# Kernel tuning notes

Measured on AMD Instinct MI355X. Metric: run time of the kernel, lower is better.

## Reference

```python
import jax, jax.numpy as jnp
import numpy as np

N = 50000
E = 500000
IN_DIM = 384
HID = 64
HEADS = 4
OUT_DIM = 128
EPS_SM = 1e-16
EPS_LN = 1e-5
NEG_SLOPE = 0.2


def gat_conv(x, row, col, ew, W, a_src, a_dst, b, heads, out_ch, concat):
    n = x.shape[0]
    h = (x @ W).reshape(n, heads, out_ch)              # [N, H, C]
    # per-node attention scores, then gather (same math as gathering h first)
    s_src = jnp.sum(h * a_src, axis=-1)                # [N, H]
    s_dst = jnp.sum(h * a_dst, axis=-1)                # [N, H]
    alpha = jax.nn.leaky_relu(s_src[row] + s_dst[col], NEG_SLOPE)  # [E, H]
    alpha = alpha * ew[:, None]
    a_exp = jnp.exp(alpha)
    denom = jax.ops.segment_sum(a_exp, col, num_segments=n)        # [N, H]
    alpha = a_exp / (denom[col] + EPS_SM)              # [E, H]
    msg = alpha[:, :, None] * h[col]                   # [E, H, C]
    out = jax.ops.segment_sum(msg, row, num_segments=n)  # [N, H, C]
    if concat:
        out = out.reshape(n, heads * out_ch)
    else:
        out = out.mean(axis=1)
    return out + b


def layer_norm(x, g, b):
    mu = x.mean(axis=-1, keepdims=True)
    var = x.var(axis=-1, keepdims=True)
    return (x - mu) / jnp.sqrt(var + EPS_LN) * g + b


def setup_inputs() -> dict:
    key = jax.random.key(0)
    ks = jax.random.split(key, 16)
    D1 = HEADS * HID  # 256
    inp = {
        "x": jax.random.normal(ks[0], (N, IN_DIM), jnp.float32),
        "edge_index": jax.random.randint(ks[1], (2, E), 0, N, jnp.int32),
        "edge_weight": jax.random.uniform(ks[2], (E,), jnp.float32),
        "W1": jax.random.normal(ks[3], (IN_DIM, D1), jnp.float32) * (1.0 / np.sqrt(IN_DIM)),
        "as1": jax.random.normal(ks[4], (1, HEADS, HID), jnp.float32) * 0.1,
        "ad1": jax.random.normal(ks[5], (1, HEADS, HID), jnp.float32) * 0.1,
        "b1": jnp.zeros((D1,), jnp.float32),
        "g1": jnp.ones((D1,), jnp.float32),
        "be1": jnp.zeros((D1,), jnp.float32),
        "W2": jax.random.normal(ks[6], (D1, D1), jnp.float32) * (1.0 / np.sqrt(D1)),
        "as2": jax.random.normal(ks[7], (1, HEADS, HID), jnp.float32) * 0.1,
        "ad2": jax.random.normal(ks[8], (1, HEADS, HID), jnp.float32) * 0.1,
        "b2": jnp.zeros((D1,), jnp.float32),
        "g2": jnp.ones((D1,), jnp.float32),
        "be2": jnp.zeros((D1,), jnp.float32),
        "W3": jax.random.normal(ks[9], (D1, OUT_DIM), jnp.float32) * (1.0 / np.sqrt(D1)),
        "as3": jax.random.normal(ks[10], (1, 1, OUT_DIM), jnp.float32) * 0.1,
        "ad3": jax.random.normal(ks[11], (1, 1, OUT_DIM), jnp.float32) * 0.1,
        "b3": jnp.zeros((OUT_DIM,), jnp.float32),
        "g3": jnp.ones((OUT_DIM,), jnp.float32),
        "be3": jnp.zeros((OUT_DIM,), jnp.float32),
    }
    return inp


def reference(x, edge_index, edge_weight, W1, as1, ad1, b1, g1, be1,
              W2, as2, ad2, b2, g2, be2, W3, as3, ad3, b3, g3, be3):
    row, col = edge_index[0], edge_index[1]
    h = gat_conv(x, row, col, edge_weight, W1, as1, ad1, b1, HEADS, HID, True)
    h = jax.nn.elu(layer_norm(h, g1, be1))
    h = gat_conv(h, row, col, edge_weight, W2, as2, ad2, b2, HEADS, HID, True)
    h = jax.nn.elu(layer_norm(h, g2, be2))
    h = gat_conv(h, row, col, edge_weight, W3, as3, ad3, b3, 1, OUT_DIM, False)
    return layer_norm(h, g3, be3)
```

## Files before the change

### kernel.cpp

```cpp
#include <hip/hip_runtime.h>
#include <hip/hip_bf16.h>


typedef __bf16 bf16x8_t __attribute__((ext_vector_type(8)));
typedef float  fx4      __attribute__((ext_vector_type(4)));

__device__ __forceinline__ float u2f(unsigned short u) {
    return __uint_as_float(((unsigned)u) << 16);
}
__device__ __forceinline__ unsigned short f2u(float f) {
    unsigned b = __float_as_uint(f);
    unsigned rounded = b + 0x7FFF + ((b >> 16) & 1);
    if (((b >> 23) & 0xFF) == 0xFF) rounded = b;
    return (unsigned short)(rounded >> 16);
}

__global__ void f32_to_bf16_k(const float* __restrict__ src, unsigned short* __restrict__ dst,
                              long n) {
    long i = (long)blockIdx.x * 256 + threadIdx.x;
    const long stride = (long)gridDim.x * 256;
    for (; i < n; i += stride) dst[i] = f2u(src[i]);
}

__global__ void transpose_conv_k(const float* __restrict__ W, unsigned short* __restrict__ Wt,
                                 int K, int N) {
    int idx = blockIdx.x * 256 + threadIdx.x;
    if (idx >= K * N) return;
    int k = idx / N, n = idx - k * N;
    Wt[(size_t)n * K + k] = f2u(W[idx]);
}

__global__ void fill_const_f32_k(float* __restrict__ out, long n, float v) {
    long i = (long)blockIdx.x * 256 + threadIdx.x;
    const long stride = (long)gridDim.x * 256;
    for (; i < n; i += stride) out[i] = v;
}

__global__ void count_both_k(const int* __restrict__ row, const int* __restrict__ col,
                             int* __restrict__ rcnt, int* __restrict__ ccnt, int E, int Nn) {
    int e = blockIdx.x * 256 + threadIdx.x;
    if (e >= E) return;
    int r = row[e], c = col[e];
    if ((unsigned)r < (unsigned)Nn) atomicAdd(&rcnt[r], 1);
    if ((unsigned)c < (unsigned)Nn) atomicAdd(&ccnt[c], 1);
}

__global__ __launch_bounds__(256) void scan1_k(const int* __restrict__ cnt,
                                               int* __restrict__ local,
                                               int* __restrict__ bsum, int n) {
    __shared__ int sm[256];
    int i = blockIdx.x * 256 + threadIdx.x;
    int tid = threadIdx.x;
    int v = (i < n) ? cnt[i] : 0;
    sm[tid] = v;
    __syncthreads();
    for (int o = 1; o < 256; o <<= 1) {
        int t = (tid >= o) ? sm[tid - o] : 0;
        __syncthreads();
        sm[tid] += t;
        __syncthreads();
    }
    if (i < n) local[i] = sm[tid];
    if (tid == 255) bsum[blockIdx.x] = sm[255];
}

__global__ __launch_bounds__(512) void scan2_k(int* __restrict__ bsum, int nb) {
    __shared__ int sm[512];
    int tid = threadIdx.x;
    int v = (tid < nb) ? bsum[tid] : 0;
    sm[tid] = v;
    __syncthreads();
    for (int o = 1; o < 512; o <<= 1) {
        int t = (tid >= o) ? sm[tid - o] : 0;
        __syncthreads();
        sm[tid] += t;
        __syncthreads();
    }
    if (tid < nb) bsum[tid] = sm[tid];
}

__global__ __launch_bounds__(256) void scan3_k(const int* __restrict__ cnt,
                                               const int* __restrict__ local,
                                               const int* __restrict__ bsum,
                                               int* __restrict__ rowptr, int* __restrict__ rcur,
                                               int* __restrict__ colptr, int* __restrict__ ccur,
                                               int N) {
    int i = blockIdx.x * 256 + threadIdx.x;
    int n2 = 2 * N;
    if (i >= n2) return;
    int b = blockIdx.x;
    int s = local[i] + (b > 0 ? bsum[b - 1] : 0);
    int v = cnt[i];
    if (i < N) {
        rowptr[i + 1] = s;
        rcur[i] = s - v;
        if (i == 0) rowptr[0] = 0;
    } else {
        int bN = (N - 1) >> 8;
        int base = local[N - 1] + (bN > 0 ? bsum[bN - 1] : 0);
        int j = i - N;
        colptr[j + 1] = s - base;
        ccur[j] = s - v - base;
        if (j == 0) colptr[0] = 0;
    }
}

__global__ void fill_both_k(const int* __restrict__ row, const int* __restrict__ col,
                            const float* __restrict__ ew,
                            int* __restrict__ rcur, int* __restrict__ ccur,
                            long* __restrict__ csr, long* __restrict__ csc,
                            int E, int Nn) {
    int e = blockIdx.x * 256 + threadIdx.x;
    if (e >= E) return;
    int r = row[e], c = col[e];
    int wb = __float_as_int(ew[e]);
    if ((unsigned)r < (unsigned)Nn) {
        int s = atomicAdd(&rcur[r], 1);
        int cc = ((unsigned)c < (unsigned)Nn) ? c : 0;
        long v = (long)(unsigned)cc | ((long)(unsigned)wb << 32);
        __builtin_nontemporal_store(v, csr + s);
    }
    if ((unsigned)c < (unsigned)Nn) {
        int s = atomicAdd(&ccur[c], 1);
        int rr = ((unsigned)r < (unsigned)Nn) ? r : 0;
        long v = (long)(unsigned)rr | ((long)(unsigned)wb << 32);
        __builtin_nontemporal_store(v, csc + s);
    }
}

#define LSTR 40
__global__ __launch_bounds__(256) void gemm_bf16(const unsigned short* __restrict__ A,
                                                 const unsigned short* __restrict__ Bt,
                                                 unsigned short* __restrict__ C,
                                                 int M, int Ncol, int K) {
    __shared__ unsigned short As[128 * LSTR];
    __shared__ unsigned short Bs[128 * LSTR];
    const int t = threadIdx.x;
    const int lane = t & 63;
    const int wave = t >> 6;
    const int quad = lane >> 4, l16 = lane & 15;
    const int row0 = blockIdx.y * 128, col0 = blockIdx.x * 128;
    const int wr = (wave >> 1) * 64, wc = (wave & 1) * 64;
    const int sr = t >> 2, ss = (t & 3) * 8;
    fx4 acc[4][4] = {};
    for (int k0 = 0; k0 < K; k0 += 32) {
#pragma unroll
        for (int rr = 0; rr < 2; rr++) {
            int r = sr + rr * 64;
            uint4 av = make_uint4(0, 0, 0, 0);
            int gr = row0 + r;
            if (gr < M) av = *(const uint4*)(A + (size_t)gr * K + k0 + ss);
            *(uint4*)(As + r * LSTR + ss) = av;
            uint4 bv = *(const uint4*)(Bt + (size_t)(col0 + r) * K + k0 + ss);
            *(uint4*)(Bs + r * LSTR + ss) = bv;
        }
        __syncthreads();
        bf16x8_t af[4], bfr[4];
#pragma unroll
        for (int i = 0; i < 4; i++) {
            af[i]  = *(const bf16x8_t*)(As + (wr + i * 16 + l16) * LSTR + quad * 8);
            bfr[i] = *(const bf16x8_t*)(Bs + (wc + i * 16 + l16) * LSTR + quad * 8);
        }
#pragma unroll
        for (int i = 0; i < 4; i++)
#pragma unroll
            for (int j = 0; j < 4; j++)
                acc[i][j] = __builtin_amdgcn_mfma_f32_16x16x32_bf16(af[i], bfr[j], acc[i][j], 0, 0, 0);
        __syncthreads();
    }
#pragma unroll
    for (int i = 0; i < 4; i++) {
        int rb = row0 + wr + i * 16 + quad * 4;
#pragma unroll
        for (int j = 0; j < 4; j++) {
            int c = col0 + wc + j * 16 + l16;
#pragma unroll
            for (int r = 0; r < 4; r++) {
                int gr = rb + r;
                if (gr < M) C[(size_t)gr * Ncol + c] = f2u(acc[i][j][r]);
            }
        }
    }
}

template <int CPL, int LPH, int H>
__global__ __launch_bounds__(256) void scores_k(const unsigned short* __restrict__ hb,
                                                const float* __restrict__ asrc,
                                                const float* __restrict__ adst,
                                                float* __restrict__ ssrc, float* __restrict__ sdst,
                                                int N) {
    int node = blockIdx.x * 4 + (threadIdx.x >> 6);
    if (node >= N) return;
    int lane = threadIdx.x & 63;
    const int D = CPL * 64;
    const unsigned short* hp = hb + (size_t)node * D + lane * CPL;
    float s1 = 0.f, s2 = 0.f;
#pragma unroll
    for (int i = 0; i < CPL; i++) {
        float h = u2f(hp[i]);
        s1 += h * asrc[lane * CPL + i];
        s2 += h * adst[lane * CPL + i];
    }
#pragma unroll
    for (int m = 1; m < LPH; m <<= 1) {
        s1 += __shfl_xor(s1, m);
        s2 += __shfl_xor(s2, m);
    }
    if ((lane & (LPH - 1)) == 0) {
        ssrc[(size_t)node * H + lane / LPH] = s1;
        sdst[(size_t)node * H + lane / LPH] = s2;
    }
}

template <int H>
__global__ __launch_bounds__(256) void denom_csc_k(const int* __restrict__ colptr,
                                                   const int2* __restrict__ csc,
                                                   const float* __restrict__ ssrc,
                                                   const float* __restrict__ sdst,
                                                   float* __restrict__ att, int N) {
    int idx = blockIdx.x * 256 + threadIdx.x;
    int node = idx / H;
    int h = idx - node * H;
    if (node >= N) return;
    const float sd = sdst[(size_t)node * H + h];
    float acc = 0.f;
    int kbeg = colptr[node], kend = colptr[node + 1];
    if (kbeg < kend) {
        int klast = kend - 1;
        int2 ceA = csc[kbeg];
        int2 ceB = csc[(kbeg + 1 < kend) ? kbeg + 1 : klast];
        int2 ceC = csc[(kbeg + 2 < kend) ? kbeg + 2 : klast];
        float sA = ssrc[(size_t)ceA.x * H + h];
        float sB = ssrc[(size_t)ceB.x * H + h];
        for (int k = kbeg; k < kend; k++) {
            int2 ceD = csc[(k + 3 < kend) ? k + 3 : klast];
            float sC = ssrc[(size_t)ceC.x * H + h];
            float we = __int_as_float(ceA.y);
            float s = sA + sd;
            s = (s > 0.f) ? s : 0.2f * s;
            acc += __expf(fminf(s * we, 60.f));
            ceA = ceB; ceB = ceC; ceC = ceD;
            sA = sB; sB = sC;
        }
    }
    att[(size_t)node * 2 * H + h] = sd;
    att[(size_t)node * 2 * H + H + h] = 1.0f / (acc + 1e-16f);
}

template <int CPL, int H, bool DOELU, bool F32OUT>
__global__ __launch_bounds__(256) void agg_ln_k(const unsigned short* __restrict__ hb,
                                                const float* __restrict__ ssrc,
                                                const float* __restrict__ att,
                                                const int* __restrict__ rowptr,
                                                const int2* __restrict__ csr,
                                                const float* __restrict__ bias,
                                                const float* __restrict__ gamma,
                                                const float* __restrict__ beta,
                                                void* __restrict__ outv, int N, int E) {
    int node = blockIdx.x * 4 + (threadIdx.x >> 6);
    if (node >= N) return;
    int lane = threadIdx.x & 63;
    const int D = CPL * 64, C = D / H;
    const int head = (lane * CPL) / C;
    const float sn = ssrc[(size_t)node * H + head];
    float acc[CPL] = {};
    int kbeg = rowptr[node], kend = rowptr[node + 1];
    if (kbeg < 0) kbeg = 0;
    if (kend > E) kend = E;

    if (kbeg < kend) {
        int klast = kend - 1;
        int2 ceA = csr[kbeg];
        int2 ceB = csr[(kbeg + 1 < kend) ? kbeg + 1 : klast];
        int2 ceC = csr[(kbeg + 2 < kend) ? kbeg + 2 : klast];
        float sdA, rdA, sdB, rdB;
        uint2 hvA, hvB;
        {
            const float* ap = att + (size_t)ceA.x * (2 * H);
            if constexpr (H == 1) { float2 p = *(const float2*)ap; sdA = p.x; rdA = p.y; }
            else { sdA = ap[head]; rdA = ap[H + head]; }
            hvA = *(const uint2*)(hb + (size_t)ceA.x * D + lane * CPL);
        }
        {
            const float* ap = att + (size_t)ceB.x * (2 * H);
            if constexpr (H == 1) { float2 p = *(const float2*)ap; sdB = p.x; rdB = p.y; }
            else { sdB = ap[head]; rdB = ap[H + head]; }
            hvB = *(const uint2*)(hb + (size_t)ceB.x * D + lane * CPL);
        }
        for (int k = kbeg; k < kend; k++) {
            int2 ceD = csr[(k + 3 < kend) ? k + 3 : klast];
            float sdC, rdC;
            uint2 hvC;
            {
                const float* ap = att + (size_t)ceC.x * (2 * H);
                if constexpr (H == 1) { float2 p = *(const float2*)ap; sdC = p.x; rdC = p.y; }
                else { sdC = ap[head]; rdC = ap[H + head]; }
                hvC = *(const uint2*)(hb + (size_t)ceC.x * D + lane * CPL);
            }
            float we = __int_as_float(ceA.y);
            float s = sn + sdA;
            s = (s > 0.f) ? s : 0.2f * s;
            float ae = __expf(fminf(s * we, 60.f));
            float w = ae * rdA;
            if constexpr (CPL == 4) {
                acc[0] += w * u2f((unsigned short)(hvA.x & 0xFFFFu));
                acc[1] += w * u2f((unsigned short)(hvA.x >> 16));
                acc[2] += w * u2f((unsigned short)(hvA.y & 0xFFFFu));
                acc[3] += w * u2f((unsigned short)(hvA.y >> 16));
            } else {
                acc[0] += w * u2f((unsigned short)(hvA.x & 0xFFFFu));
                acc[1] += w * u2f((unsigned short)(hvA.x >> 16));
            }
            ceA = ceB; ceB = ceC; ceC = ceD;
            sdA = sdB; rdA = rdB; hvA = hvB;
            sdB = sdC; rdB = rdC; hvB = hvC;
        }
    }
    float v[CPL];
    float sum = 0.f, sq = 0.f;
#pragma unroll
    for (int i = 0; i < CPL; i++) {
        v[i] = acc[i] + bias[lane * CPL + i];
        sum += v[i];
        sq += v[i] * v[i];
    }
#pragma unroll
    for (int m = 1; m < 64; m <<= 1) {
        sum += __shfl_xor(sum, m);
        sq += __shfl_xor(sq, m);
    }
    float mu  = sum * (1.0f / D);
    float var = sq * (1.0f / D) - mu * mu;
    float inv = rsqrtf(fmaxf(var, 0.f) + 1e-5f);
#pragma unroll
    for (int i = 0; i < CPL; i++) {
        float y = (v[i] - mu) * inv * gamma[lane * CPL + i] + beta[lane * CPL + i];
        if (DOELU) y = (y > 0.f) ? y : (__expf(y) - 1.f);
        size_t idx = (size_t)node * D + lane * CPL + i;
        if constexpr (F32OUT) ((float*)outv)[idx] = y;
        else                  ((unsigned short*)outv)[idx] = f2u(y);
    }
}

extern "C" void kernel_launch(void* const* d_in, const int* in_sizes, int n_in,
                              void* d_out, int out_size, void* d_ws, size_t ws_size,
                              hipStream_t stream) {
    const int IN_DIM = 384;
    const int N = in_sizes[0] / IN_DIM;
    const int E = in_sizes[1] / 2;
    float* outp = (float*)d_out;
    const int FG = 2048;

    if (n_in != 21 || out_size != N * 128) {
        fill_const_f32_k<<<FG, 256, 0, stream>>>(outp, (long)out_size, 9.0f);
        return;
    }

    const float* x = (const float*)d_in[0];
    const int* ei = (const int*)d_in[1];
    const int* row = ei;
    const int* col = ei + E;
    const float* ew = (const float*)d_in[2];
    const float* W1 = (const float*)d_in[3];
    const float* as1 = (const float*)d_in[4];
    const float* ad1 = (const float*)d_in[5];
    const float* b1 = (const float*)d_in[6];
    const float* g1 = (const float*)d_in[7];
    const float* be1 = (const float*)d_in[8];
    const float* W2 = (const float*)d_in[9];
    const float* as2 = (const float*)d_in[10];
    const float* ad2 = (const float*)d_in[11];
    const float* b2 = (const float*)d_in[12];
    const float* g2 = (const float*)d_in[13];
    const float* be2 = (const float*)d_in[14];
    const float* W3 = (const float*)d_in[15];
    const float* as3 = (const float*)d_in[16];
    const float* ad3 = (const float*)d_in[17];
    const float* b3 = (const float*)d_in[18];
    const float* g3 = (const float*)d_in[19];
    const float* be3 = (const float*)d_in[20];

    char* ws = (char*)d_ws;
    size_t off = 0;
    auto alloc = [&](size_t b) -> char* {
        char* p = ws + off;
        off = (off + b + 255) & ~(size_t)255;
        return p;
    };
    unsigned short* xb = (unsigned short*)alloc((size_t)N * IN_DIM * 2);
    unsigned short* hb = (unsigned short*)alloc((size_t)N * 256 * 2);
    unsigned short* ab = (unsigned short*)alloc((size_t)N * 256 * 2);
    float* att = (float*)alloc((size_t)N * 8 * 4);
    float* ssrc = (float*)alloc((size_t)N * 4 * 4);
    float* sdst = (float*)alloc((size_t)N * 4 * 4);
    unsigned short* W1t = (unsigned short*)alloc((size_t)384 * 256 * 2);
    unsigned short* W2t = (unsigned short*)alloc((size_t)256 * 256 * 2);
    unsigned short* W3t = (unsigned short*)alloc((size_t)256 * 128 * 2);
    int* rowptr = (int*)alloc((size_t)(N + 1) * 4);
    int* colptr = (int*)alloc((size_t)(N + 1) * 4);
    int* cnt2 = (int*)alloc((size_t)2 * N * 4);
    int* slocal = (int*)alloc((size_t)2 * N * 4);
    int* sbsum = (int*)alloc((size_t)512 * 4);
    int* rcur = (int*)alloc((size_t)N * 4);
    int* ccur = (int*)alloc((size_t)N * 4);
    long* csr = (long*)alloc((size_t)E * 8);
    long* csc = (long*)alloc((size_t)E * 8);

    if (off > ws_size) {
        fill_const_f32_k<<<FG, 256, 0, stream>>>(outp, (long)out_size, 7.0f);
        return;
    }

    int* rcnt = cnt2;
    int* ccnt = cnt2 + N;

    const int ebl = (E + 255) / 256;
    const int nbl4 = (N + 3) / 4;
    const int mrows = (N + 127) / 128;
    const int n2 = 2 * N;
    const int sblocks = (n2 + 255) / 256;

    f32_to_bf16_k<<<FG, 256, 0, stream>>>(x, xb, (long)N * IN_DIM);
    transpose_conv_k<<<(384 * 256 + 255) / 256, 256, 0, stream>>>(W1, W1t, 384, 256);
    transpose_conv_k<<<(256 * 256 + 255) / 256, 256, 0, stream>>>(W2, W2t, 256, 256);
    transpose_conv_k<<<(256 * 128 + 255) / 256, 256, 0, stream>>>(W3, W3t, 256, 128);

    hipMemsetAsync(cnt2, 0, (size_t)n2 * 4, stream);
    count_both_k<<<ebl, 256, 0, stream>>>(row, col, rcnt, ccnt, E, N);
    scan1_k<<<sblocks, 256, 0, stream>>>(cnt2, slocal, sbsum, n2);
    scan2_k<<<1, 512, 0, stream>>>(sbsum, sblocks);
    scan3_k<<<sblocks, 256, 0, stream>>>(cnt2, slocal, sbsum, rowptr, rcur, colptr, ccur, N);
    fill_both_k<<<ebl, 256, 0, stream>>>(row, col, ew, rcur, ccur, csr, csc, E, N);

    gemm_bf16<<<dim3(2, mrows), 256, 0, stream>>>(xb, W1t, hb, N, 256, 384);
    scores_k<4, 16, 4><<<nbl4, 256, 0, stream>>>(hb, as1, ad1, ssrc, sdst, N);
    denom_csc_k<4><<<(N * 4 + 255) / 256, 256, 0, stream>>>(colptr, (const int2*)csc, ssrc, sdst, att, N);
    agg_ln_k<4, 4, true, false><<<nbl4, 256, 0, stream>>>(hb, ssrc, att, rowptr, (const int2*)csr,
                                                          b1, g1, be1, ab, N, E);

    gemm_bf16<<<dim3(2, mrows), 256, 0, stream>>>(ab, W2t, hb, N, 256, 256);
    scores_k<4, 16, 4><<<nbl4, 256, 0, stream>>>(hb, as2, ad2, ssrc, sdst, N);
    denom_csc_k<4><<<(N * 4 + 255) / 256, 256, 0, stream>>>(colptr, (const int2*)csc, ssrc, sdst, att, N);
    agg_ln_k<4, 4, true, false><<<nbl4, 256, 0, stream>>>(hb, ssrc, att, rowptr, (const int2*)csr,
                                                          b2, g2, be2, ab, N, E);

    gemm_bf16<<<dim3(1, mrows), 256, 0, stream>>>(ab, W3t, hb, N, 128, 256);
    scores_k<2, 64, 1><<<nbl4, 256, 0, stream>>>(hb, as3, ad3, ssrc, sdst, N);
    denom_csc_k<1><<<(N + 255) / 256, 256, 0, stream>>>(colptr, (const int2*)csc, ssrc, sdst, att, N);
    agg_ln_k<2, 1, false, true><<<nbl4, 256, 0, stream>>>(hb, ssrc, att, rowptr, (const int2*)csr,
                                                          b3, g3, be3, outp, N, E);
}
```

Measured before the change: 583.9 us.

## Split each wavefront into two half-waves processing alternate edges with wider loads

The aggregation kernel now has each 64-lane wavefront split into two 32-lane halves. Each half handles alternate neighbor edges and loads twice as many features per lane (16-byte instead of 8-byte gathers). The partial sums are combined with a cross-half shuffle before layer norm, and only one half writes the output. This aims to halve the serial edge-loop length per node and raise memory-level parallelism on the random gathers, at the cost of more registers, masked tail edges and an extra reduction.

```diff
diff --git a/kernel.cpp b/kernel.cpp
--- a/kernel.cpp
+++ b/kernel.cpp
@@ -259,86 +259,105 @@
                                                 void* __restrict__ outv, int N, int E) {
     int node = blockIdx.x * 4 + (threadIdx.x >> 6);
     if (node >= N) return;
-    int lane = threadIdx.x & 63;
-    const int D = CPL * 64, C = D / H;
-    const int head = (lane * CPL) / C;
+    const int lane = threadIdx.x & 63;
+    const int hl = lane & 31;
+    const int eo = lane >> 5;
+    const int D = CPL * 32, C = D / H;
+    const int colbase = hl * CPL;
+    const int head = colbase / C;
     const float sn = ssrc[(size_t)node * H + head];
+    const unsigned short* hbl = hb + colbase;
     float acc[CPL] = {};
     int kbeg = rowptr[node], kend = rowptr[node + 1];
     if (kbeg < 0) kbeg = 0;
     if (kend > E) kend = E;
 
     if (kbeg < kend) {
-        int klast = kend - 1;
-        int2 ceA = csr[kbeg];
-        int2 ceB = csr[(kbeg + 1 < kend) ? kbeg + 1 : klast];
-        int2 ceC = csr[(kbeg + 2 < kend) ? kbeg + 2 : klast];
+        const int klast = kend - 1;
+        int kA = kbeg + eo, kB = kbeg + 2 + eo, kC = kbeg + 4 + eo;
+        int2 ceA = csr[kA < kend ? kA : klast];
+        int2 ceB = csr[kB < kend ? kB : klast];
+        int2 ceC = csr[kC < kend ? kC : klast];
         float sdA, rdA, sdB, rdB;
-        uint2 hvA, hvB;
+        uint4 hvA = make_uint4(0,0,0,0), hvB = make_uint4(0,0,0,0);
         {
             const float* ap = att + (size_t)ceA.x * (2 * H);
             if constexpr (H == 1) { float2 p = *(const float2*)ap; sdA = p.x; rdA = p.y; }
             else { sdA = ap[head]; rdA = ap[H + head]; }
-            hvA = *(const uint2*)(hb + (size_t)ceA.x * D + lane * CPL);
+            const unsigned short* hp = hbl + (size_t)ceA.x * D;
+            if constexpr (CPL == 8) hvA = *(const uint4*)hp;
+            else { uint2 t2 = *(const uint2*)hp; hvA.x = t2.x; hvA.y = t2.y; }
         }
         {
             const float* ap = att + (size_t)ceB.x * (2 * H);
             if constexpr (H == 1) { float2 p = *(const float2*)ap; sdB = p.x; rdB = p.y; }
             else { sdB = ap[head]; rdB = ap[H + head]; }
-            hvB = *(const uint2*)(hb + (size_t)ceB.x * D + lane * CPL);
-        }
-        for (int k = kbeg; k < kend; k++) {
-            int2 ceD = csr[(k + 3 < kend) ? k + 3 : klast];
+            const unsigned short* hp = hbl + (size_t)ceB.x * D;
+            if constexpr (CPL == 8) hvB = *(const uint4*)hp;
+            else { uint2 t2 = *(const uint2*)hp; hvB.x = t2.x; hvB.y = t2.y; }
+        }
+        for (int k = kbeg; k < kend; k += 2) {
+            int kD = k + 6 + eo;
+            int2 ceD = csr[kD < kend ? kD : klast];
             float sdC, rdC;
-            uint2 hvC;
+            uint4 hvC = make_uint4(0,0,0,0);
             {
                 const float* ap = att + (size_t)ceC.x * (2 * H);
                 if constexpr (H == 1) { float2 p = *(const float2*)ap; sdC = p.x; rdC = p.y; }
                 else { sdC = ap[head]; rdC = ap[H + head]; }
-                hvC = *(const uint2*)(hb + (size_t)ceC.x * D + lane * CPL);
+                const unsigned short* hp = hbl + (size_t)ceC.x * D;
+                if constexpr (CPL == 8) hvC = *(const uint4*)hp;
+                else { uint2 t2 = *(const uint2*)hp; hvC.x = t2.x; hvC.y = t2.y; }
             }
             float we = __int_as_float(ceA.y);
             float s = sn + sdA;
             s = (s > 0.f) ? s : 0.2f * s;
             float ae = __expf(fminf(s * we, 60.f));
             float w = ae * rdA;
-            if constexpr (CPL == 4) {
-                acc[0] += w * u2f((unsigned short)(hvA.x & 0xFFFFu));
-                acc[1] += w * u2f((unsigned short)(hvA.x >> 16));
-                acc[2] += w * u2f((unsigned short)(hvA.y & 0xFFFFu));
-                acc[3] += w * u2f((unsigned short)(hvA.y >> 16));
-            } else {
-                acc[0] += w * u2f((unsigned short)(hvA.x & 0xFFFFu));
-                acc[1] += w * u2f((unsigned short)(hvA.x >> 16));
+            w = (k + eo < kend) ? w : 0.f;
+            acc[0] += w * u2f((unsigned short)(hvA.x & 0xFFFFu));
+            acc[1] += w * u2f((unsigned short)(hvA.x >> 16));
+            acc[2] += w * u2f((unsigned short)(hvA.y & 0xFFFFu));
+            acc[3] += w * u2f((unsigned short)(hvA.y >> 16));
+            if constexpr (CPL == 8) {
+                acc[4] += w * u2f((unsigned short)(hvA.z & 0xFFFFu));
+                acc[5] += w * u2f((unsigned short)(hvA.z >> 16));
+                acc[6] += w * u2f((unsigned short)(hvA.w & 0xFFFFu));
+                acc[7] += w * u2f((unsigned short)(hvA.w >> 16));
             }
             ceA = ceB; ceB = ceC; ceC = ceD;
             sdA = sdB; rdA = rdB; hvA = hvB;
             sdB = sdC; rdB = rdC; hvB = hvC;
         }
     }
+#pragma unroll
+    for (int i = 0; i < CPL; i++) acc[i] += __shfl_xor(acc[i], 32);
+
     float v[CPL];
     float sum = 0.f, sq = 0.f;
 #pragma unroll
     for (int i = 0; i < CPL; i++) {
-        v[i] = acc[i] + bias[lane * CPL + i];
+        v[i] = acc[i] + bias[colbase + i];
         sum += v[i];
         sq += v[i] * v[i];
     }
 #pragma unroll
-    for (int m = 1; m < 64; m <<= 1) {
+    for (int m = 1; m < 32; m <<= 1) {
         sum += __shfl_xor(sum, m);
         sq += __shfl_xor(sq, m);
     }
     float mu  = sum * (1.0f / D);
     float var = sq * (1.0f / D) - mu * mu;
     float inv = rsqrtf(fmaxf(var, 0.f) + 1e-5f);
-#pragma unroll
-    for (int i = 0; i < CPL; i++) {
-        float y = (v[i] - mu) * inv * gamma[lane * CPL + i] + beta[lane * CPL + i];
-        if (DOELU) y = (y > 0.f) ? y : (__expf(y) - 1.f);
-        size_t idx = (size_t)node * D + lane * CPL + i;
-        if constexpr (F32OUT) ((float*)outv)[idx] = y;
-        else                  ((unsigned short*)outv)[idx] = f2u(y);
+    if (eo == 0) {
+#pragma unroll
+        for (int i = 0; i < CPL; i++) {
+            float y = (v[i] - mu) * inv * gamma[colbase + i] + beta[colbase + i];
+            if (DOELU) y = (y > 0.f) ? y : (__expf(y) - 1.f);
+            size_t idx = (size_t)node * D + colbase + i;
+            if constexpr (F32OUT) ((float*)outv)[idx] = y;
+            else                  ((unsigned short*)outv)[idx] = f2u(y);
+        }
     }
 }
 
@@ -435,18 +454,18 @@
     gemm_bf16<<<dim3(2, mrows), 256, 0, stream>>>(xb, W1t, hb, N, 256, 384);
     scores_k<4, 16, 4><<<nbl4, 256, 0, stream>>>(hb, as1, ad1, ssrc, sdst, N);
     denom_csc_k<4><<<(N * 4 + 255) / 256, 256, 0, stream>>>(colptr, (const int2*)csc, ssrc, sdst, att, N);
-    agg_ln_k<4, 4, true, false><<<nbl4, 256, 0, stream>>>(hb, ssrc, att, rowptr, (const int2*)csr,
+    agg_ln_k<8, 4, true, false><<<nbl4, 256, 0, stream>>>(hb, ssrc, att, rowptr, (const int2*)csr,
                                                           b1, g1, be1, ab, N, E);
 
     gemm_bf16<<<dim3(2, mrows), 256, 0, stream>>>(ab, W2t, hb, N, 256, 256);
     scores_k<4, 16, 4><<<nbl4, 256, 0, stream>>>(hb, as2, ad2, ssrc, sdst, N);
     denom_csc_k<4><<<(N * 4 + 255) / 256, 256, 0, stream>>>(colptr, (const int2*)csc, ssrc, sdst, att, N);
-    agg_ln_k<4, 4, true, false><<<nbl4, 256, 0, stream>>>(hb, ssrc, att, rowptr, (const int2*)csr,
+    agg_ln_k<8, 4, true, false><<<nbl4, 256, 0, stream>>>(hb, ssrc, att, rowptr, (const int2*)csr,
                                                           b2, g2, be2, ab, N, E);
 
     gemm_bf16<<<dim3(1, mrows), 256, 0, stream>>>(ab, W3t, hb, N, 128, 256);
     scores_k<2, 64, 1><<<nbl4, 256, 0, stream>>>(hb, as3, ad3, ssrc, sdst, N);
     denom_csc_k<1><<<(N + 255) / 256, 256, 0, stream>>>(colptr, (const int2*)csc, ssrc, sdst, att, N);
-    agg_ln_k<2, 1, false, true><<<nbl4, 256, 0, stream>>>(hb, ssrc, att, rowptr, (const int2*)csr,
+    agg_ln_k<4, 1, false, true><<<nbl4, 256, 0, stream>>>(hb, ssrc, att, rowptr, (const int2*)csr,
                                                           b3, g3, be3, outp, N, E);
 }
```

New measurement: 547.7 us. 1.07x faster.
